# Kernel optimization log

Measured on AMD Instinct MI355X. Metric: run time of the kernel, lower is better.

Reference implementation:

```python
import jax, jax.numpy as jnp
import numpy as np

B = 131072   # batch_sz
NB = 3       # n_blocks (n_agents)
SS = 16      # single_state
NA = 9       # n_action
VD = 128     # vector_dim
CM = 10      # confidence_mid_dim
EPS = 1e-8   # torch CosineSimilarity eps


def _linear_params(k, out_d, in_d):
    bound = 1.0 / np.sqrt(in_d)
    kw, kb = jax.random.split(k)
    W = jax.random.uniform(kw, (out_d, in_d), minval=-bound, maxval=bound, dtype=jnp.float32)
    b = jax.random.uniform(kb, (out_d,), minval=-bound, maxval=bound, dtype=jnp.float32)
    return W, b


def setup_inputs() -> dict:
    key = jax.random.key(0)
    ks = jax.random.split(key, 11)
    Wq, bq = _linear_params(ks[0], VD, SS + NA)
    Wk, bk = _linear_params(ks[1], VD, SS + NA)
    Wv, bv = _linear_params(ks[2], VD, SS + NA)
    W1, b1 = _linear_params(ks[3], VD, VD)
    W2, b2 = _linear_params(ks[4], SS, VD)
    Wc1, bc1 = _linear_params(ks[5], CM, NB * (SS + NA))
    Wc2, bc2 = _linear_params(ks[6], 3, CM)
    states = jax.random.normal(ks[7], (B, NB, SS), dtype=jnp.float32)
    action = jax.random.normal(ks[8], (B, NA), dtype=jnp.float32)
    block_id = jax.random.randint(ks[9], (B, NB), 0, 2, dtype=jnp.int32)
    return {
        'states': states, 'action': action, 'block_id': block_id,
        'Wq': Wq, 'bq': bq, 'Wk': Wk, 'bk': bk, 'Wv': Wv, 'bv': bv,
        'W1': W1, 'b1': b1, 'W2': W2, 'b2': b2,
        'Wc1': Wc1, 'bc1': bc1, 'Wc2': Wc2, 'bc2': bc2,
    }


def reference(states, action, block_id, Wq, bq, Wk, bk, Wv, bv, W1, b1, W2, b2, Wc1, bc1, Wc2, bc2):
    # create_block_action: broadcast action over blocks, mask non-selected blocks to -1
    act = jnp.where(block_id[:, :, None] == 1, action[:, None, :], -1.0)  # [B,NB,NA]
    ba = jnp.concatenate([states, act], axis=-1)                          # [B,NB,SS+NA]

    # QKV projections (fused over blocks instead of per-block loop)
    q = ba @ Wq.T + bq   # [B,NB,VD]
    k = ba @ Wk.T + bk
    v = ba @ Wv.T + bv

    # cosine-similarity attention: d[b,i,j] = cos(q[b,i], k[b,j])
    num = jnp.einsum('bid,bjd->bij', q, k)                                # [B,NB,NB]
    qn = jnp.linalg.norm(q, axis=-1)                                      # [B,NB]
    kn = jnp.linalg.norm(k, axis=-1)
    d = num / jnp.maximum(qn[:, :, None] * kn[:, None, :], EPS)
    a = jax.nn.softmax(d, axis=2)

    res = jnp.einsum('bij,bjd->bid', a, v)                                # [B,NB,VD]
    res = jnp.tanh(res @ W1.T + b1)
    res = res @ W2.T + b2                                                 # [B,NB,SS]
    res = res.reshape(B, 1, NB * SS)

    flat = ba.reshape(B, 1, NB * (SS + NA))                               # [B,1,75]
    conf = jax.nn.sigmoid(jax.nn.sigmoid(flat @ Wc1.T + bc1) @ Wc2.T + bc2)  # [B,1,3]

    residuals = jnp.concatenate([res, conf], axis=-1)                     # [B,1,51]
    base = jnp.concatenate(
        [states.reshape(B, 1, NB * SS), jnp.zeros((B, 1, 3), dtype=states.dtype)], axis=-1)
    return base + residuals
```

## Files before the change

kernel.cpp:

```cpp
#include <hip/hip_runtime.h>
#include <math.h>

#define BTOT 131072
#define NBK 3
#define SS 16
#define NA 9
#define BAD 25
#define STR 28
#define VD 128
#define CM 10
#define OUTD 51
#define EPS 1e-8f

#define O_GQK  0
#define O_GQQ  700
#define O_GKK  1400
#define O_V1   2100
#define O_V2   2128
#define O_VQ   2156
#define O_VK   2184
#define O_C    2212
#define O_M    2216
#define O_B2   7976
#define O_WC1  7992
#define O_BC1  8832
#define O_WC2  8844
#define O_BC2  8880
#define LDS_F  8884
#define O_PKM  LDS_F
#define O_PKW2 (LDS_F + 2048)
#define PKM_N  4096
#define PKW2_N 2048

#define NDOT  (O_M + PKM_N)
#define NCOPY (16 + 840 + 12 + 36 + 4 + PKW2_N)

typedef __attribute__((ext_vector_type(8))) short short8;
typedef __attribute__((ext_vector_type(4))) float floatx4;
typedef __attribute__((ext_vector_type(2))) float float2v;

__device__ __forceinline__ float fast_sigmoid(float x) {
    return __builtin_amdgcn_rcpf(1.0f + __expf(-x));
}

__device__ __forceinline__ unsigned short f2bf(float f) {
    unsigned int u = __float_as_uint(f);
    u += 0x7FFFu + ((u >> 16) & 1u);
    return (unsigned short)(u >> 16);
}

__device__ __forceinline__ float2v pk_fma(float2v a, float2v b, float2v c) {
    float2v d;
    asm("v_pk_fma_f32 %0, %1, %2, %3" : "=v"(d) : "v"(a), "v"(b), "v"(c));
    return d;
}
__device__ __forceinline__ float2v pk_mul(float2v a, float2v b) {
    float2v d;
    asm("v_pk_mul_f32 %0, %1, %2" : "=v"(d) : "v"(a), "v"(b));
    return d;
}
__device__ __forceinline__ unsigned int cvt_pk_bf16(float lo, float hi) {
    unsigned int r;
    asm("v_cvt_pk_bf16_f32 %0, %1, %2" : "=v"(r) : "v"(lo), "v"(hi));
    return r;
}

__global__ __launch_bounds__(256) void prep_dots(
    const float* __restrict__ Wq, const float* __restrict__ bq,
    const float* __restrict__ Wk, const float* __restrict__ bk,
    const float* __restrict__ Wv, const float* __restrict__ bv,
    const float* __restrict__ W1, const float* __restrict__ b1,
    float* __restrict__ ws) {
    int lane = threadIdx.x & 63;
    int gidx = blockIdx.x * 4 + (threadIdx.x >> 6);
    if (gidx >= NDOT) return;

    const float* pa = bq;  const float* pb = bk;
    int sa = 1, sb = 1;
    float scale = 1.0f, bias = 0.0f;
    bool zero = false;
    bool isbf = false; int bfpos = 0;

    if (gidx < O_M) {
        int idx = gidx;
        if (idx < O_GQQ) {
            int e = idx / STR, f = idx % STR;
            if (f < BAD) { pa = Wq + e; sa = BAD; pb = Wk + f; sb = BAD; }
            else zero = true;
        } else if (idx < O_GKK) {
            int j = idx - O_GQQ; int e = j / STR, f = j % STR;
            if (f < BAD && f <= e) { pa = Wq + e; sa = BAD; pb = Wq + f; sb = BAD; scale = (f == e) ? 1.0f : 2.0f; }
            else zero = true;
        } else if (idx < O_V1) {
            int j = idx - O_GKK; int e = j / STR, f = j % STR;
            if (f < BAD && f <= e) { pa = Wk + e; sa = BAD; pb = Wk + f; sb = BAD; scale = (f == e) ? 1.0f : 2.0f; }
            else zero = true;
        } else if (idx < O_V2) {
            int e = idx - O_V1;
            if (e < BAD) { pa = Wq + e; sa = BAD; pb = bk; }
            else zero = true;
        } else if (idx < O_VQ) {
            int e = idx - O_V2;
            if (e < BAD) { pa = Wk + e; sa = BAD; pb = bq; }
            else zero = true;
        } else if (idx < O_VK) {
            int e = idx - O_VQ;
            if (e < BAD) { pa = Wq + e; sa = BAD; pb = bq; }
            else zero = true;
        } else if (idx < O_C) {
            int e = idx - O_VK;
            if (e < BAD) { pa = Wk + e; sa = BAD; pb = bk; }
            else zero = true;
        } else {
            int j = idx - O_C;
            if (j == 0)      { pa = bq; pb = bk; }
            else if (j == 1) { pa = bq; pb = bq; }
            else if (j == 2) { pa = bk; pb = bk; }
            else zero = true;
        }
    } else {
        int p = gidx - O_M;
        isbf = true; bfpos = p;
        int l2 = (p >> 3) & 63, j = p & 7;
        int n = (p >> 9) * 16 + (l2 & 15);
        int k = ((l2 >> 4) << 3) + j;
        if (k < BAD)       { pa = W1 + n * VD; pb = Wv + k; sb = BAD; scale = 2.0f; }
        else if (k == BAD) { pa = W1 + n * VD; pb = bv; scale = 2.0f; bias = 2.0f * b1[n]; }
        else zero = true;
    }

    float s = 0.0f;
    if (!zero)
        s = pa[sa * lane] * pb[sb * lane] + pa[sa * (lane + 64)] * pb[sb * (lane + 64)];
    #pragma unroll
    for (int off = 1; off < 64; off <<= 1) s += __shfl_xor(s, off);
    float val = zero ? 0.0f : (s * scale + bias);
    if (lane == 0) {
        if (isbf) ((unsigned short*)(ws + O_PKM))[bfpos] = f2bf(val);
        else ws[gidx] = val;
    }
}

__global__ __launch_bounds__(256) void prep_copy(
    const float* __restrict__ W2, const float* __restrict__ b2,
    const float* __restrict__ Wc1, const float* __restrict__ bc1,
    const float* __restrict__ Wc2, const float* __restrict__ bc2,
    float* __restrict__ ws) {
    int c = blockIdx.x * 256 + threadIdx.x;
    if (c >= NCOPY) return;
    if (c < 16) { ws[O_B2 + c] = b2[c]; return; }
    c -= 16;
    if (c < 840) {
        int m = c / 84, r = c % 84, i = r / STR, f = r % STR;
        ws[O_WC1 + c] = (f < BAD) ? Wc1[m * (NBK * BAD) + i * BAD + f] : 0.0f;
        return;
    }
    c -= 840;
    if (c < 12) { ws[O_BC1 + c] = (c < CM) ? bc1[c] : 0.0f; return; }
    c -= 12;
    if (c < 36) { int o = c / 12, mm = c % 12; ws[O_WC2 + c] = (mm < CM) ? Wc2[o * CM + mm] : 0.0f; return; }
    c -= 36;
    if (c < 4) { ws[O_BC2 + c] = (c < 3) ? bc2[c] : 0.0f; return; }
    c -= 4;
    int kt = c >> 9, l = (c >> 3) & 63, j = c & 7;
    int o = l & 15;
    int k = kt * 32 + ((l >> 4) << 3) + j;
    ((unsigned short*)(ws + O_PKW2))[c] = f2bf(W2[o * VD + k]);
}

__global__ __launch_bounds__(256) void main_kernel(
    const float* __restrict__ states, const float* __restrict__ action,
    const int* __restrict__ block_id,
    const float* __restrict__ ws, float* __restrict__ out) {
    __shared__ __align__(16) unsigned short At[384 * 40];

    int t = threadIdx.x;
    int lane = t & 63;
    int h = t & 1;
    int le = t >> 1;
    long elem = (long)blockIdx.x * 128 + le;

    const float* st = states + elem * (NBK * SS);
    const float* ac = action + elem * NA;
    const int* bid = block_id + elem * NBK;

    float2v ba2[NBK][13];
    #pragma unroll
    for (int i = 0; i < NBK; ++i) {
        const float4* s4 = (const float4*)(st + i * SS);
        float4 v0 = s4[0], v1 = s4[1], v2 = s4[2], v3 = s4[3];
        ba2[i][0] = float2v{v0.x, v0.y}; ba2[i][1] = float2v{v0.z, v0.w};
        ba2[i][2] = float2v{v1.x, v1.y}; ba2[i][3] = float2v{v1.z, v1.w};
        ba2[i][4] = float2v{v2.x, v2.y}; ba2[i][5] = float2v{v2.z, v2.w};
        ba2[i][6] = float2v{v3.x, v3.y}; ba2[i][7] = float2v{v3.z, v3.w};
        bool sel = (bid[i] == 1);
        float av[9];
        #pragma unroll
        for (int c = 0; c < 9; ++c) av[c] = sel ? ac[c] : -1.0f;
        ba2[i][8]  = float2v{av[0], av[1]};
        ba2[i][9]  = float2v{av[2], av[3]};
        ba2[i][10] = float2v{av[4], av[5]};
        ba2[i][11] = float2v{av[6], av[7]};
        ba2[i][12] = float2v{av[8], 0.0f};
    }

    {
        const float* wc = ws + O_WC1 + h * 5 * 84;
        const float* bc = ws + O_BC1 + h * 5;
        float hp[5];
        #pragma unroll
        for (int k = 0; k < 5; ++k) {
            float2v a2 = {0.f, 0.f};
            #pragma unroll
            for (int i = 0; i < NBK; ++i) {
                const float2v* w2 = (const float2v*)(wc + k * 84 + i * STR);
                #pragma unroll
                for (int p = 0; p < 13; ++p) a2 = pk_fma(w2[p], ba2[i][p], a2);
            }
            hp[k] = fast_sigmoid(bc[k] + a2.x + a2.y);
        }
        float op5[5];
        #pragma unroll
        for (int k = 0; k < 5; ++k) op5[k] = __shfl_xor(hp[k], 1);
        if (h == 0) {
            float* op = out + elem * OUTD;
            #pragma unroll
            for (int o = 0; o < 3; ++o) {
                float s = ws[O_BC2 + o];
                #pragma unroll
                for (int m = 0; m < 5; ++m) s += ws[O_WC2 + o * 12 + m] * hp[m];
                #pragma unroll
                for (int m = 0; m < 5; ++m) s += ws[O_WC2 + o * 12 + 5 + m] * op5[m];
                op[48 + o] = fast_sigmoid(s);
            }
        }
    }

    float sl[NBK], dd[NBK];
    {
        const float2v* vA2 = (const float2v*)(ws + (h ? O_V2 : O_V1));
        const float2v* vB2 = (const float2v*)(ws + (h ? O_VK : O_VQ));
        #pragma unroll
        for (int p = 0; p < NBK; ++p) {
            float2v sA = {0.f, 0.f}, sB = {0.f, 0.f};
            #pragma unroll
            for (int k = 0; k < 13; ++k) {
                sA = pk_fma(vA2[k], ba2[p][k], sA);
                sB = pk_fma(vB2[k], ba2[p][k], sB);
            }
            sl[p] = sA.x + sA.y; dd[p] = sB.x + sB.y;
        }
    }

    float nm[NBK][NBK] = {{0.f,0.f,0.f},{0.f,0.f,0.f},{0.f,0.f,0.f}};
    {
        const float* gq = ws + O_GQK + h * STR;
        #pragma unroll
        for (int i13 = 0; i13 < 13; ++i13) {
            const float* grow = (i13 == 12) ? (ws + O_GQK + 24 * STR)
                                            : (gq + i13 * 2 * STR);
            const float2v* g2 = (const float2v*)grow;
            float2v t20 = {0.f, 0.f}, t21 = {0.f, 0.f}, t22 = {0.f, 0.f};
            #pragma unroll
            for (int p = 0; p < 13; ++p) {
                t20 = pk_fma(g2[p], ba2[0][p], t20);
                t21 = pk_fma(g2[p], ba2[1][p], t21);
                t22 = pk_fma(g2[p], ba2[2][p], t22);
            }
            float t0 = t20.x + t20.y, t1 = t21.x + t21.y, t2s = t22.x + t22.y;
            #pragma unroll
            for (int i = 0; i < NBK; ++i) {
                float be;
                if (i13 == 12) be = ba2[i][12].x * (1.0f - (float)h);
                else           be = h ? ba2[i][i13].y : ba2[i][i13].x;
                nm[i][0] = fmaf(be, t0, nm[i][0]);
                nm[i][1] = fmaf(be, t1, nm[i][1]);
                nm[i][2] = fmaf(be, t2s, nm[i][2]);
            }
        }
        #pragma unroll
        for (int i = 0; i < NBK; ++i)
            #pragma unroll
            for (int j = 0; j < NBK; ++j)
                nm[i][j] += __shfl_xor(nm[i][j], 1);
    }

    float rn[NBK];
    {
        const float* gt = ws + (h ? O_GKK : O_GQQ);
        float sn2[NBK] = {0.f, 0.f, 0.f};
        #pragma unroll
        for (int e = 0; e < BAD; ++e) {
            const float2v* g2 = (const float2v*)(gt + e * STR);
            float2v q20 = {0.f, 0.f}, q21 = {0.f, 0.f}, q22 = {0.f, 0.f};
            #pragma unroll
            for (int k = 0; k < (e + 1) / 2; ++k) {
                q20 = pk_fma(g2[k], ba2[0][k], q20);
                q21 = pk_fma(g2[k], ba2[1][k], q21);
                q22 = pk_fma(g2[k], ba2[2][k], q22);
            }
            float p0 = q20.x + q20.y, p1 = q21.x + q21.y, p2 = q22.x + q22.y;
            if ((e & 1) == 0) {
                float g = gt[e * STR + e];
                p0 = fmaf(g, ba2[0][e / 2].x, p0);
                p1 = fmaf(g, ba2[1][e / 2].x, p1);
                p2 = fmaf(g, ba2[2][e / 2].x, p2);
            }
            float be0 = (e & 1) ? ba2[0][e / 2].y : ba2[0][e / 2].x;
            float be1 = (e & 1) ? ba2[1][e / 2].y : ba2[1][e / 2].x;
            float be2 = (e & 1) ? ba2[2][e / 2].y : ba2[2][e / 2].x;
            sn2[0] = fmaf(be0, p0, sn2[0]);
            sn2[1] = fmaf(be1, p1, sn2[1]);
            sn2[2] = fmaf(be2, p2, sn2[2]);
        }
        float cc = ws[O_C + 1 + h];
        #pragma unroll
        for (int p = 0; p < NBK; ++p) {
            sn2[p] += 2.0f * dd[p] + cc;
            rn[p] = __builtin_amdgcn_sqrtf(fmaxf(sn2[p], 0.0f));
        }
    }

    float orn[NBK], osl[NBK];
    #pragma unroll
    for (int p = 0; p < NBK; ++p) {
        orn[p] = __shfl_xor(rn[p], 1);
        osl[p] = __shfl_xor(sl[p], 1);
    }
    float s1v[NBK], s2v[NBK], qv[NBK], kv[NBK];
    #pragma unroll
    for (int p = 0; p < NBK; ++p) {
        s1v[p] = h ? osl[p] : sl[p];
        s2v[p] = h ? sl[p] : osl[p];
        qv[p]  = h ? orn[p] : rn[p];
        kv[p]  = h ? rn[p] : orn[p];
    }
    float c0 = ws[O_C + 0];

    float att[NBK][NBK];
    #pragma unroll
    for (int i = 0; i < NBK; ++i) {
        float dv[NBK];
        #pragma unroll
        for (int j = 0; j < NBK; ++j)
            dv[j] = (nm[i][j] + s1v[i] + s2v[j] + c0) *
                    __builtin_amdgcn_rcpf(fmaxf(qv[i] * kv[j], EPS));
        float mx = fmaxf(dv[0], fmaxf(dv[1], dv[2]));
        float e0 = __expf(dv[0] - mx);
        float e1 = __expf(dv[1] - mx);
        float e2 = __expf(dv[2] - mx);
        float inv = __builtin_amdgcn_rcpf(e0 + e1 + e2);
        att[i][0] = e0 * inv;
        att[i][1] = e1 * inv;
        att[i][2] = e2 * inv;
    }

    #pragma unroll
    for (int i = 0; i < NBK; ++i) {
        unsigned int* dst = (unsigned int*)&At[(le * 3 + i) * 40];
        float2v w0 = {att[i][0], att[i][0]};
        float2v w1 = {att[i][1], att[i][1]};
        float2v w2d = {att[i][2], att[i][2]};
        #pragma unroll
        for (int d = 0; d < 6; ++d) {
            float2v va = pk_fma(ba2[0][d], w0, pk_fma(ba2[1][d], w1, pk_mul(ba2[2][d], w2d)));
            float2v vb = pk_fma(ba2[0][6 + d], w0, pk_fma(ba2[1][6 + d], w1, pk_mul(ba2[2][6 + d], w2d)));
            float lo = h ? vb.x : va.x;
            float hi = h ? vb.y : va.y;
            dst[h * 6 + d] = cvt_pk_bf16(lo, hi);
        }
        if (h) {
            float v24 = ba2[0][12].x * att[i][0] + ba2[1][12].x * att[i][1] + ba2[2][12].x * att[i][2];
            dst[12] = cvt_pk_bf16(v24, 1.0f);
        } else {
            dst[13] = 0u; dst[14] = 0u; dst[15] = 0u;
        }
    }

    asm volatile("s_waitcnt lgkmcnt(0)" ::: "memory");

    {
        int w = t >> 6;
        int m = lane & 15, q = lane >> 4;
        const short8* pkM = (const short8*)(ws + O_PKM);
        const short8* pkW2 = (const short8*)(ws + O_PKW2);
        float b2v = ws[O_B2 + m];
        long blockbase = (long)blockIdx.x * 128;
        int addrA = ((q & 1) ? (m + 32) : m) << 2;
        int addrB = addrA + 64;
        bool hiSel = (q >= 2);

        for (int tt = 0; tt < 6; ++tt) {
            int tile = w * 6 + tt;
            short8 af = *(const short8*)&At[(tile * 16 + m) * 40 + q * 8];
            floatx4 accT[8];
            #pragma unroll
            for (int nt = 0; nt < 8; ++nt) {
                floatx4 z = {0.f, 0.f, 0.f, 0.f};
                accT[nt] = __builtin_amdgcn_mfma_f32_16x16x32_bf16(pkM[nt * 64 + lane], af, z, 0, 0, 0);
            }
            unsigned int pk[8][2];
            #pragma unroll
            for (int nt = 0; nt < 8; ++nt) {
                float x0 = fmaf(-2.0f, __builtin_amdgcn_rcpf(1.0f + __expf(accT[nt][0])), 1.0f);
                float x1 = fmaf(-2.0f, __builtin_amdgcn_rcpf(1.0f + __expf(accT[nt][1])), 1.0f);
                float x2 = fmaf(-2.0f, __builtin_amdgcn_rcpf(1.0f + __expf(accT[nt][2])), 1.0f);
                float x3 = fmaf(-2.0f, __builtin_amdgcn_rcpf(1.0f + __expf(accT[nt][3])), 1.0f);
                pk[nt][0] = cvt_pk_bf16(x0, x1);
                pk[nt][1] = cvt_pk_bf16(x2, x3);
            }
            floatx4 acc2 = {0.f, 0.f, 0.f, 0.f};
            #pragma unroll
            for (int kt = 0; kt < 4; ++kt) {
                int lo0 = __builtin_amdgcn_ds_bpermute(addrA, (int)pk[2 * kt][0]);
                int hi0 = __builtin_amdgcn_ds_bpermute(addrA, (int)pk[2 * kt + 1][0]);
                int lo1 = __builtin_amdgcn_ds_bpermute(addrA, (int)pk[2 * kt][1]);
                int hi1 = __builtin_amdgcn_ds_bpermute(addrA, (int)pk[2 * kt + 1][1]);
                int lo2 = __builtin_amdgcn_ds_bpermute(addrB, (int)pk[2 * kt][0]);
                int hi2 = __builtin_amdgcn_ds_bpermute(addrB, (int)pk[2 * kt + 1][0]);
                int lo3 = __builtin_amdgcn_ds_bpermute(addrB, (int)pk[2 * kt][1]);
                int hi3 = __builtin_amdgcn_ds_bpermute(addrB, (int)pk[2 * kt + 1][1]);
                union { unsigned int u[4]; short8 s; } a2u;
                a2u.u[0] = (unsigned int)(hiSel ? hi0 : lo0);
                a2u.u[1] = (unsigned int)(hiSel ? hi1 : lo1);
                a2u.u[2] = (unsigned int)(hiSel ? hi2 : lo2);
                a2u.u[3] = (unsigned int)(hiSel ? hi3 : lo3);
                acc2 = __builtin_amdgcn_mfma_f32_16x16x32_bf16(a2u.s, pkW2[kt * 64 + lane], acc2, 0, 0, 0);
            }
            #pragma unroll
            for (int rr = 0; rr < 4; ++rr) {
                int lrow = tile * 16 + q * 4 + rr;
                int et = lrow / 3, i = lrow - et * 3;
                long ge = blockbase + et;
                float base = states[ge * 48 + i * 16 + m];
                out[ge * OUTD + i * 16 + m] = acc2[rr] + base + b2v;
            }
        }
    }
}

extern "C" void kernel_launch(void* const* d_in, const int* in_sizes, int n_in,
                              void* d_out, int out_size, void* d_ws, size_t ws_size,
                              hipStream_t stream) {
    const float* states = (const float*)d_in[0];
    const float* action = (const float*)d_in[1];
    const int* block_id = (const int*)d_in[2];
    const float* Wq = (const float*)d_in[3];
    const float* bq = (const float*)d_in[4];
    const float* Wk = (const float*)d_in[5];
    const float* bk = (const float*)d_in[6];
    const float* Wv = (const float*)d_in[7];
    const float* bv = (const float*)d_in[8];
    const float* W1 = (const float*)d_in[9];
    const float* b1 = (const float*)d_in[10];
    const float* W2 = (const float*)d_in[11];
    const float* b2 = (const float*)d_in[12];
    const float* Wc1 = (const float*)d_in[13];
    const float* bc1 = (const float*)d_in[14];
    const float* Wc2 = (const float*)d_in[15];
    const float* bc2 = (const float*)d_in[16];
    float* out = (float*)d_out;
    float* ws = (float*)d_ws;

    hipLaunchKernelGGL(prep_dots, dim3((NDOT + 3) / 4), dim3(256), 0, stream,
                       Wq, bq, Wk, bk, Wv, bv, W1, b1, ws);
    hipLaunchKernelGGL(prep_copy, dim3((NCOPY + 255) / 256), dim3(256), 0, stream,
                       W2, b2, Wc1, bc1, Wc2, bc2, ws);
    hipLaunchKernelGGL(main_kernel, dim3(BTOT / 128), dim3(256), 0, stream,
                       states, action, block_id, ws, out);
}
```

Before: 169.7 us.

## Split each batch element across four lanes instead of two

Each batch element is now handled by four threads instead of two, so each block covers 64 elements and the grid doubles. The per-element Gram-form dot products, norms, confidence MLP and attention-weighted value rows are divided four ways, with partial results combined through DPP broadcasts and xor shuffles. This cuts the serial VALU work per thread and raises parallelism. In exchange it adds more cross-lane reductions, redundant input loads per element, and fewer MFMA tiles per wave, which amortise the weight fragment loads less well.

```diff
diff --git a/kernel.cpp b/kernel.cpp
--- a/kernel.cpp
+++ b/kernel.cpp
@@ -65,6 +65,11 @@
     return r;
 }
 
+#define QB0(x) __int_as_float(__builtin_amdgcn_mov_dpp(__float_as_int(x), 0x00, 0xF, 0xF, false))
+#define QB1(x) __int_as_float(__builtin_amdgcn_mov_dpp(__float_as_int(x), 0x55, 0xF, 0xF, false))
+#define QB2(x) __int_as_float(__builtin_amdgcn_mov_dpp(__float_as_int(x), 0xAA, 0xF, 0xF, false))
+#define QB3(x) __int_as_float(__builtin_amdgcn_mov_dpp(__float_as_int(x), 0xFF, 0xF, 0xF, false))
+
 __global__ __launch_bounds__(256) void prep_dots(
     const float* __restrict__ Wq, const float* __restrict__ bq,
     const float* __restrict__ Wk, const float* __restrict__ bk,
@@ -172,13 +177,13 @@
     const float* __restrict__ states, const float* __restrict__ action,
     const int* __restrict__ block_id,
     const float* __restrict__ ws, float* __restrict__ out) {
-    __shared__ __align__(16) unsigned short At[384 * 40];
+    __shared__ __align__(16) unsigned short At[192 * 40];
 
     int t = threadIdx.x;
     int lane = t & 63;
-    int h = t & 1;
-    int le = t >> 1;
-    long elem = (long)blockIdx.x * 128 + le;
+    int p4 = t & 3;
+    int le = t >> 2;
+    long elem = (long)blockIdx.x * 64 + le;
 
     const float* st = states + elem * (NBK * SS);
     const float* ac = action + elem * NA;
@@ -204,12 +209,109 @@
         ba2[i][12] = float2v{av[8], 0.0f};
     }
 
-    {
-        const float* wc = ws + O_WC1 + h * 5 * 84;
-        const float* bc = ws + O_BC1 + h * 5;
-        float hp[5];
-        #pragma unroll
-        for (int k = 0; k < 5; ++k) {
+    float vecd[NBK];
+    {
+        const float2v* v2 = (const float2v*)(ws + O_V1 + p4 * STR);
+        #pragma unroll
+        for (int p = 0; p < NBK; ++p) {
+            float2v a = {0.f, 0.f};
+            #pragma unroll
+            for (int k = 0; k < 13; ++k) a = pk_fma(v2[k], ba2[p][k], a);
+            vecd[p] = a.x + a.y;
+        }
+    }
+    float s1b[NBK], s2b[NBK], dqb[NBK], dkb[NBK];
+    #pragma unroll
+    for (int p = 0; p < NBK; ++p) {
+        s1b[p] = QB0(vecd[p]);
+        s2b[p] = QB1(vecd[p]);
+        dqb[p] = QB2(vecd[p]);
+        dkb[p] = QB3(vecd[p]);
+    }
+
+    float rn[NBK], qv[NBK], kv[NBK];
+    {
+        const float* gt = ws + (p4 >= 2 ? O_GKK : O_GQQ) + (p4 & 1) * STR;
+        bool odd = (p4 & 1);
+        float sn2p[NBK] = {0.f, 0.f, 0.f};
+        #pragma unroll
+        for (int ii = 0; ii < 13; ++ii) {
+            const float2v* g2 = (const float2v*)(gt + ii * 2 * STR);
+            float2v a0 = {0.f, 0.f}, a1 = {0.f, 0.f}, a2 = {0.f, 0.f};
+            #pragma unroll
+            for (int k = 0; k <= ii; ++k) {
+                a0 = pk_fma(g2[k], ba2[0][k], a0);
+                a1 = pk_fma(g2[k], ba2[1][k], a1);
+                a2 = pk_fma(g2[k], ba2[2][k], a2);
+            }
+            float p0 = a0.x + a0.y, p1 = a1.x + a1.y, p2 = a2.x + a2.y;
+            float be0 = odd ? ba2[0][ii].y : ba2[0][ii].x;
+            float be1 = odd ? ba2[1][ii].y : ba2[1][ii].x;
+            float be2 = odd ? ba2[2][ii].y : ba2[2][ii].x;
+            sn2p[0] = fmaf(be0, p0, sn2p[0]);
+            sn2p[1] = fmaf(be1, p1, sn2p[1]);
+            sn2p[2] = fmaf(be2, p2, sn2p[2]);
+        }
+        float cq = ws[O_C + 1], ck = ws[O_C + 2];
+        float cc = (p4 < 2) ? cq : ck;
+        #pragma unroll
+        for (int p = 0; p < NBK; ++p) {
+            float sn2 = sn2p[p] + __shfl_xor(sn2p[p], 1);
+            float dv2 = (p4 < 2) ? dqb[p] : dkb[p];
+            sn2 += 2.0f * dv2 + cc;
+            rn[p] = __builtin_amdgcn_sqrtf(fmaxf(sn2, 0.0f));
+            float orn = __shfl_xor(rn[p], 2);
+            qv[p] = (p4 < 2) ? rn[p] : orn;
+            kv[p] = (p4 < 2) ? orn : rn[p];
+        }
+    }
+
+    float nm[NBK][NBK] = {{0.f,0.f,0.f},{0.f,0.f,0.f},{0.f,0.f,0.f}};
+    {
+        const float* gq = ws + O_GQK + p4 * STR;
+        bool oddp = (p4 & 1), hip = (p4 & 2);
+        #pragma unroll
+        for (int ii = 0; ii < 7; ++ii) {
+            const float2v* g2 = (const float2v*)(gq + ii * 4 * STR);
+            float2v t20 = {0.f, 0.f}, t21 = {0.f, 0.f}, t22 = {0.f, 0.f};
+            #pragma unroll
+            for (int k = 0; k < 13; ++k) {
+                t20 = pk_fma(g2[k], ba2[0][k], t20);
+                t21 = pk_fma(g2[k], ba2[1][k], t21);
+                t22 = pk_fma(g2[k], ba2[2][k], t22);
+            }
+            float t0 = t20.x + t20.y, t1 = t21.x + t21.y, t2s = t22.x + t22.y;
+            #pragma unroll
+            for (int i = 0; i < NBK; ++i) {
+                float be;
+                if (ii < 6) {
+                    float c01 = oddp ? ba2[i][2 * ii].y     : ba2[i][2 * ii].x;
+                    float c23 = oddp ? ba2[i][2 * ii + 1].y : ba2[i][2 * ii + 1].x;
+                    be = hip ? c23 : c01;
+                } else {
+                    be = (p4 == 0) ? ba2[i][12].x : 0.0f;
+                }
+                nm[i][0] = fmaf(be, t0, nm[i][0]);
+                nm[i][1] = fmaf(be, t1, nm[i][1]);
+                nm[i][2] = fmaf(be, t2s, nm[i][2]);
+            }
+        }
+        #pragma unroll
+        for (int i = 0; i < NBK; ++i)
+            #pragma unroll
+            for (int j = 0; j < NBK; ++j) {
+                nm[i][j] += __shfl_xor(nm[i][j], 1);
+                nm[i][j] += __shfl_xor(nm[i][j], 2);
+            }
+    }
+
+    {
+        int mstart = (p4 <= 2) ? 3 * p4 : 8;
+        const float* wc = ws + O_WC1 + mstart * 84;
+        const float* bc = ws + O_BC1 + mstart;
+        float hp[3];
+        #pragma unroll
+        for (int k = 0; k < 3; ++k) {
             float2v a2 = {0.f, 0.f};
             #pragma unroll
             for (int i = 0; i < NBK; ++i) {
@@ -219,160 +321,68 @@
             }
             hp[k] = fast_sigmoid(bc[k] + a2.x + a2.y);
         }
-        float op5[5];
-        #pragma unroll
-        for (int k = 0; k < 5; ++k) op5[k] = __shfl_xor(hp[k], 1);
-        if (h == 0) {
+        float po[3];
+        #pragma unroll
+        for (int o = 0; o < 3; ++o) {
+            const float* w2r = ws + O_WC2 + o * 12 + mstart;
+            float s = w2r[0] * hp[0] + w2r[1] * hp[1];
+            float w3 = (p4 < 2) ? w2r[2] : 0.0f;
+            s = fmaf(w3, hp[2], s);
+            po[o] = s;
+        }
+        #pragma unroll
+        for (int o = 0; o < 3; ++o) {
+            po[o] += __shfl_xor(po[o], 1);
+            po[o] += __shfl_xor(po[o], 2);
+        }
+        if (p4 == 0) {
             float* op = out + elem * OUTD;
             #pragma unroll
-            for (int o = 0; o < 3; ++o) {
-                float s = ws[O_BC2 + o];
-                #pragma unroll
-                for (int m = 0; m < 5; ++m) s += ws[O_WC2 + o * 12 + m] * hp[m];
-                #pragma unroll
-                for (int m = 0; m < 5; ++m) s += ws[O_WC2 + o * 12 + 5 + m] * op5[m];
-                op[48 + o] = fast_sigmoid(s);
-            }
-        }
-    }
-
-    float sl[NBK], dd[NBK];
-    {
-        const float2v* vA2 = (const float2v*)(ws + (h ? O_V2 : O_V1));
-        const float2v* vB2 = (const float2v*)(ws + (h ? O_VK : O_VQ));
-        #pragma unroll
-        for (int p = 0; p < NBK; ++p) {
-            float2v sA = {0.f, 0.f}, sB = {0.f, 0.f};
-            #pragma unroll
-            for (int k = 0; k < 13; ++k) {
-                sA = pk_fma(vA2[k], ba2[p][k], sA);
-                sB = pk_fma(vB2[k], ba2[p][k], sB);
-            }
-            sl[p] = sA.x + sA.y; dd[p] = sB.x + sB.y;
-        }
-    }
-
-    float nm[NBK][NBK] = {{0.f,0.f,0.f},{0.f,0.f,0.f},{0.f,0.f,0.f}};
-    {
-        const float* gq = ws + O_GQK + h * STR;
-        #pragma unroll
-        for (int i13 = 0; i13 < 13; ++i13) {
-            const float* grow = (i13 == 12) ? (ws + O_GQK + 24 * STR)
-                                            : (gq + i13 * 2 * STR);
-            const float2v* g2 = (const float2v*)grow;
-            float2v t20 = {0.f, 0.f}, t21 = {0.f, 0.f}, t22 = {0.f, 0.f};
-            #pragma unroll
-            for (int p = 0; p < 13; ++p) {
-                t20 = pk_fma(g2[p], ba2[0][p], t20);
-                t21 = pk_fma(g2[p], ba2[1][p], t21);
-                t22 = pk_fma(g2[p], ba2[2][p], t22);
-            }
-            float t0 = t20.x + t20.y, t1 = t21.x + t21.y, t2s = t22.x + t22.y;
-            #pragma unroll
-            for (int i = 0; i < NBK; ++i) {
-                float be;
-                if (i13 == 12) be = ba2[i][12].x * (1.0f - (float)h);
-                else           be = h ? ba2[i][i13].y : ba2[i][i13].x;
-                nm[i][0] = fmaf(be, t0, nm[i][0]);
-                nm[i][1] = fmaf(be, t1, nm[i][1]);
-                nm[i][2] = fmaf(be, t2s, nm[i][2]);
-            }
-        }
-        #pragma unroll
-        for (int i = 0; i < NBK; ++i)
+            for (int o = 0; o < 3; ++o)
+                op[48 + o] = fast_sigmoid(po[o] + ws[O_BC2 + o]);
+        }
+    }
+
+    float att[NBK][NBK];
+    {
+        float c0 = ws[O_C + 0];
+        #pragma unroll
+        for (int i = 0; i < NBK; ++i) {
+            float dv[NBK];
             #pragma unroll
             for (int j = 0; j < NBK; ++j)
-                nm[i][j] += __shfl_xor(nm[i][j], 1);
-    }
-
-    float rn[NBK];
-    {
-        const float* gt = ws + (h ? O_GKK : O_GQQ);
-        float sn2[NBK] = {0.f, 0.f, 0.f};
-        #pragma unroll
-        for (int e = 0; e < BAD; ++e) {
-            const float2v* g2 = (const float2v*)(gt + e * STR);
-            float2v q20 = {0.f, 0.f}, q21 = {0.f, 0.f}, q22 = {0.f, 0.f};
-            #pragma unroll
-            for (int k = 0; k < (e + 1) / 2; ++k) {
-                q20 = pk_fma(g2[k], ba2[0][k], q20);
-                q21 = pk_fma(g2[k], ba2[1][k], q21);
-                q22 = pk_fma(g2[k], ba2[2][k], q22);
-            }
-            float p0 = q20.x + q20.y, p1 = q21.x + q21.y, p2 = q22.x + q22.y;
-            if ((e & 1) == 0) {
-                float g = gt[e * STR + e];
-                p0 = fmaf(g, ba2[0][e / 2].x, p0);
-                p1 = fmaf(g, ba2[1][e / 2].x, p1);
-                p2 = fmaf(g, ba2[2][e / 2].x, p2);
-            }
-            float be0 = (e & 1) ? ba2[0][e / 2].y : ba2[0][e / 2].x;
-            float be1 = (e & 1) ? ba2[1][e / 2].y : ba2[1][e / 2].x;
-            float be2 = (e & 1) ? ba2[2][e / 2].y : ba2[2][e / 2].x;
-            sn2[0] = fmaf(be0, p0, sn2[0]);
-            sn2[1] = fmaf(be1, p1, sn2[1]);
-            sn2[2] = fmaf(be2, p2, sn2[2]);
-        }
-        float cc = ws[O_C + 1 + h];
-        #pragma unroll
-        for (int p = 0; p < NBK; ++p) {
-            sn2[p] += 2.0f * dd[p] + cc;
-            rn[p] = __builtin_amdgcn_sqrtf(fmaxf(sn2[p], 0.0f));
-        }
-    }
-
-    float orn[NBK], osl[NBK];
-    #pragma unroll
-    for (int p = 0; p < NBK; ++p) {
-        orn[p] = __shfl_xor(rn[p], 1);
-        osl[p] = __shfl_xor(sl[p], 1);
-    }
-    float s1v[NBK], s2v[NBK], qv[NBK], kv[NBK];
-    #pragma unroll
-    for (int p = 0; p < NBK; ++p) {
-        s1v[p] = h ? osl[p] : sl[p];
-        s2v[p] = h ? sl[p] : osl[p];
-        qv[p]  = h ? orn[p] : rn[p];
-        kv[p]  = h ? rn[p] : orn[p];
-    }
-    float c0 = ws[O_C + 0];
-
-    float att[NBK][NBK];
-    #pragma unroll
-    for (int i = 0; i < NBK; ++i) {
-        float dv[NBK];
-        #pragma unroll
-        for (int j = 0; j < NBK; ++j)
-            dv[j] = (nm[i][j] + s1v[i] + s2v[j] + c0) *
-                    __builtin_amdgcn_rcpf(fmaxf(qv[i] * kv[j], EPS));
-        float mx = fmaxf(dv[0], fmaxf(dv[1], dv[2]));
-        float e0 = __expf(dv[0] - mx);
-        float e1 = __expf(dv[1] - mx);
-        float e2 = __expf(dv[2] - mx);
-        float inv = __builtin_amdgcn_rcpf(e0 + e1 + e2);
-        att[i][0] = e0 * inv;
-        att[i][1] = e1 * inv;
-        att[i][2] = e2 * inv;
-    }
-
-    #pragma unroll
-    for (int i = 0; i < NBK; ++i) {
-        unsigned int* dst = (unsigned int*)&At[(le * 3 + i) * 40];
-        float2v w0 = {att[i][0], att[i][0]};
-        float2v w1 = {att[i][1], att[i][1]};
-        float2v w2d = {att[i][2], att[i][2]};
-        #pragma unroll
-        for (int d = 0; d < 6; ++d) {
-            float2v va = pk_fma(ba2[0][d], w0, pk_fma(ba2[1][d], w1, pk_mul(ba2[2][d], w2d)));
-            float2v vb = pk_fma(ba2[0][6 + d], w0, pk_fma(ba2[1][6 + d], w1, pk_mul(ba2[2][6 + d], w2d)));
-            float lo = h ? vb.x : va.x;
-            float hi = h ? vb.y : va.y;
-            dst[h * 6 + d] = cvt_pk_bf16(lo, hi);
-        }
-        if (h) {
-            float v24 = ba2[0][12].x * att[i][0] + ba2[1][12].x * att[i][1] + ba2[2][12].x * att[i][2];
+                dv[j] = (nm[i][j] + s1b[i] + s2b[j] + c0) *
+                        __builtin_amdgcn_rcpf(fmaxf(qv[i] * kv[j], EPS));
+            float mx = fmaxf(dv[0], fmaxf(dv[1], dv[2]));
+            float e0 = __expf(dv[0] - mx);
+            float e1 = __expf(dv[1] - mx);
+            float e2 = __expf(dv[2] - mx);
+            float inv = __builtin_amdgcn_rcpf(e0 + e1 + e2);
+            att[i][0] = e0 * inv;
+            att[i][1] = e1 * inv;
+            att[i][2] = e2 * inv;
+        }
+    }
+
+    {
+        float aw[NBK];
+        #pragma unroll
+        for (int j = 0; j < NBK; ++j) {
+            float a01 = (p4 & 1) ? att[1][j] : att[0][j];
+            aw[j] = (p4 >= 2) ? att[2][j] : a01;
+        }
+        int irow = (p4 < 2) ? p4 : 2;
+        unsigned int* dst = (unsigned int*)&At[(le * 3 + irow) * 40];
+        bool stq = (p4 < 3);
+        float2v w0 = {aw[0], aw[0]}, w1 = {aw[1], aw[1]}, w2d = {aw[2], aw[2]};
+        #pragma unroll
+        for (int pr = 0; pr < 12; ++pr) {
+            float2v v = pk_fma(ba2[0][pr], w0, pk_fma(ba2[1][pr], w1, pk_mul(ba2[2][pr], w2d)));
+            if (stq) dst[pr] = cvt_pk_bf16(v.x, v.y);
+        }
+        float v24 = ba2[0][12].x * aw[0] + ba2[1][12].x * aw[1] + ba2[2][12].x * aw[2];
+        if (stq) {
             dst[12] = cvt_pk_bf16(v24, 1.0f);
-        } else {
             dst[13] = 0u; dst[14] = 0u; dst[15] = 0u;
         }
     }
@@ -385,13 +395,13 @@
         const short8* pkM = (const short8*)(ws + O_PKM);
         const short8* pkW2 = (const short8*)(ws + O_PKW2);
         float b2v = ws[O_B2 + m];
-        long blockbase = (long)blockIdx.x * 128;
+        long blockbase = (long)blockIdx.x * 64;
         int addrA = ((q & 1) ? (m + 32) : m) << 2;
         int addrB = addrA + 64;
         bool hiSel = (q >= 2);
 
-        for (int tt = 0; tt < 6; ++tt) {
-            int tile = w * 6 + tt;
+        for (int tt = 0; tt < 3; ++tt) {
+            int tile = w * 3 + tt;
             short8 af = *(const short8*)&At[(tile * 16 + m) * 40 + q * 8];
             floatx4 accT[8];
             #pragma unroll
@@ -466,6 +476,6 @@
                        Wq, bq, Wk, bk, Wv, bv, W1, b1, ws);
     hipLaunchKernelGGL(prep_copy, dim3((NCOPY + 255) / 256), dim3(256), 0, stream,
                        W2, b2, Wc1, bc1, Wc2, bc2, ws);
-    hipLaunchKernelGGL(main_kernel, dim3(BTOT / 128), dim3(256), 0, stream,
+    hipLaunchKernelGGL(main_kernel, dim3(BTOT / 64), dim3(256), 0, stream,
                        states, action, block_id, ws, out);
 }
```

New measurement: 225.1 us. 1.33x slower.
